# Performance work log

Hardware: AMD Instinct MI355X
Metric: run time of the kernel (lower is better)

## Reference

```python
import jax, jax.numpy as jnp
import numpy as np

N, C, T, V = 32, 64, 512, 25
CO = 64            # out_channels
C4 = CO // 4       # inter channel (conv_a/conv_d output, kc//3)
W3 = 3 * V         # unfolded node dim
BN_EPS = 1e-5


def setup_inputs() -> dict:
    key = jax.random.key(0)
    ks = jax.random.split(key, 12)
    s = 0.05
    return {
        "x": jax.random.normal(ks[0], (N, C, T, V), dtype=jnp.float32),
        "A": jax.random.uniform(ks[1], (3, W3, W3), dtype=jnp.float32) * 0.1,  # fixed adjacency buffer
        "PA": jnp.full((3, W3, W3), 1e-6, dtype=jnp.float32),                   # learned adjacency offset
        "conv_a_w": jax.random.normal(ks[2], (C4, C), dtype=jnp.float32) * s,   # 1x1 conv_a[0]
        "conv_a_b": jnp.zeros((C4,), dtype=jnp.float32),
        "conv_d_w": jax.random.normal(ks[3], (C4, C), dtype=jnp.float32) * s,   # 1x1 conv_d[0]
        "conv_d_b": jnp.zeros((C4,), dtype=jnp.float32),
        "conv_w": jax.random.normal(ks[4], (3 * C4, C), dtype=jnp.float32) * s, # main 1x1 conv (t_kernel_size=1)
        "conv_b": jnp.zeros((3 * C4,), dtype=jnp.float32),
        "out_w": jax.random.normal(ks[5], (CO, C4, 3), dtype=jnp.float32) * s,  # conv3d kernel (1,3,1)
        "out_b": jnp.zeros((CO,), dtype=jnp.float32),
        "bn_gamma": jnp.ones((CO,), dtype=jnp.float32),
        "bn_beta": jnp.zeros((CO,), dtype=jnp.float32),
        "bn_mean": jnp.zeros((CO,), dtype=jnp.float32),
        "bn_var": jnp.ones((CO,), dtype=jnp.float32),
    }


def _unfold3(x):
    # UnfoldTemporalWindows(3,1,1): (N,C,T,V) -> (N,C,T,3V), zero-pad T by 1
    n, c, t, v = x.shape
    xp = jnp.pad(x, ((0, 0), (0, 0), (1, 1), (0, 0)))
    win = jnp.stack([xp[:, :, i:i + t, :] for i in range(3)], axis=3)  # (N,C,T,3,V)
    return win.reshape(n, c, t, 3 * v)


def reference(x, A, PA, conv_a_w, conv_a_b, conv_d_w, conv_d_b,
              conv_w, conv_b, out_w, out_b, bn_gamma, bn_beta, bn_mean, bn_var):
    n, c, t, v = x.shape
    w3 = 3 * v
    Aeff = A + PA  # (3, 3V, 3V)

    x2 = _unfold3(x)  # (N,C,T,3V)

    # adaptive graph attention: matmul-softmax-matmul
    a1 = jnp.einsum('nctw,oc->notw', x2, conv_a_w) + conv_a_b[None, :, None, None]  # (N,C4,T,3V)
    a11 = a1.transpose(0, 3, 1, 2).reshape(n, w3, -1)   # (N,3V,C4*T)
    a2 = a1.reshape(n, -1, w3)                          # (N,C4*T,3V)
    att = jax.nn.softmax(jnp.matmul(a11, a2) / w3, axis=-2)  # (N,3V,3V), softmax over dim -2
    xz = jnp.matmul(x2.reshape(n, c * t, w3), att).reshape(n, c, t, w3)
    z = jnp.einsum('nctw,oc->notw', xz, conv_d_w) + conv_d_b[None, :, None, None]  # (N,C4,T,3V)

    # main branch: 1x1 conv -> split into k=3 -> einsum graph conv with A
    x1 = jnp.einsum('nctw,oc->notw', x2, conv_w) + conv_b[None, :, None, None]  # (N,3*C4,T,3V)
    c4 = conv_d_w.shape[0]
    x1 = x1.reshape(n, 3, c4, t, w3)
    x1 = jnp.einsum('nkctv,kvw->nctw', x1, Aeff)  # (N,C4,T,3V)
    x1 = x1 + z

    # conv3d (1,3,1) collapses the window-of-3 dim
    x1 = x1.reshape(n, c4, t, 3, v)
    y = jnp.einsum('nctwv,ocw->notv', x1, out_w) + out_b[None, :, None, None]  # (N,CO,T,V)

    # BatchNorm2d (inference form)
    inv = jax.lax.rsqrt(bn_var + BN_EPS)
    y = (y - bn_mean[None, :, None, None]) * (bn_gamma * inv)[None, :, None, None] + bn_beta[None, :, None, None]

    y = y + x  # in_channels == out_channels -> identity residual
    return jax.nn.relu(y)
```

## Files before the change

### kernel.cpp

```cpp
#include <hip/hip_runtime.h>
#include <hip/hip_bf16.h>


typedef unsigned short u16;
typedef unsigned int   u32;
typedef __attribute__((ext_vector_type(8))) short bf16x8;
typedef __attribute__((ext_vector_type(4))) float f32x4;

__device__ __forceinline__ float b2f(u32 u) {
    union { u32 i; float f; } x; x.i = (u & 0xffffu) << 16; return x.f;
}
__device__ __forceinline__ u16 f2b(float f) {
    union { float f; u32 i; } x; x.f = f;
    u32 i = x.i;
    return (u16)((i + 0x7fffu + ((i >> 16) & 1u)) >> 16);
}
__device__ __forceinline__ u32 pack2(float a, float b) {
    return (u32)f2b(a) | ((u32)f2b(b) << 16);
}

__global__ __launch_bounds__(256) void k0_bta(
    const float* __restrict__ A, const float* __restrict__ PA,
    u16* __restrict__ BtA)
{
    int e = blockIdx.x * 256 + threadIdx.x;
    if (e >= 80 * 288) return;
    int w = e / 288, k = e - w * 288;
    int r = k >> 5, v = k & 31, g = r / 3, i = r - g * 3;
    float val = 0.f;
    if (v < 25 && w < 75) {
        int idx = (g * 75 + i * 25 + v) * 75 + w;
        val = A[idx] + PA[idx];
    }
    BtA[e] = f2b(val);
}

__global__ __launch_bounds__(256, 2) void k1_conv80(
    const float* __restrict__ x,
    const float* __restrict__ wa, const float* __restrict__ ba,
    const float* __restrict__ wd, const float* __restrict__ bd,
    const float* __restrict__ wc, const float* __restrict__ bc,
    u16* __restrict__ a1o, u16* __restrict__ hcn)
{
    __shared__ __align__(16) u16 Xt[256 * 64];
    __shared__ __align__(16) u16 Csh[80 * 264];
    char* XtB = (char*)Xt;

    const int b    = blockIdx.x;
    const int n    = b >> 4;
    const int t0   = (b & 15) << 5;
    const int tid  = threadIdx.x;
    const int wave = tid >> 6, lane = tid & 63;
    const int q    = lane >> 4, r = lane & 15;

    bf16x8 wfrag[5][2];
    float  breg[5];
    #pragma unroll
    for (int mt = 0; mt < 5; ++mt) {
        const int o = mt * 16 + r;
        const float* src = (o < 16) ? (wa + o * 64)
                         : (o < 32) ? (wd + (o - 16) * 64)
                                    : (wc + (o - 32) * 64);
        breg[mt] = (o < 16) ? ba[o] : (o < 32) ? bd[o - 16] : bc[o - 32];
        #pragma unroll
        for (int ks = 0; ks < 2; ++ks) {
            bf16x8 f;
            #pragma unroll
            for (int j = 0; j < 8; ++j)
                f[j] = (short)f2b(src[ks * 32 + q * 8 + j]);
            wfrag[mt][ks] = f;
        }
    }

    if (t0 == 0) {
        uint4 z; z.x = 0u; z.y = 0u; z.z = 0u; z.w = 0u;
        for (int e = tid; e < 50; e += 256)
            *(uint4*)&a1o[((size_t)n * 514) * 400 + e * 8] = z;
    }
    if (t0 == 480) {
        uint4 z; z.x = 0u; z.y = 0u; z.z = 0u; z.w = 0u;
        for (int e = tid; e < 50; e += 256)
            *(uint4*)&a1o[((size_t)n * 514 + 513) * 400 + e * 8] = z;
    }

    {
        uint4 z; z.x = 0u; z.y = 0u; z.z = 0u; z.w = 0u;
        for (int e = tid; e < 448; e += 256) {
            const int pc = e >> 3, ch = e & 7;
            const int tl = pc / 7, pv = pc - tl * 7;
            const int col = tl * 32 + 25 + pv;
            *(uint4*)(XtB + col * 128 + ch * 16) = z;
        }
    }

    auto epilogue = [&](int tbp) {
        for (int e = tid; e < 2048; e += 256) {
            const int tl  = e >> 8;
            const int rem = e & 255;
            const int cc  = rem >> 2, v0 = (rem & 3) << 3;
            const int o   = (cc < 48) ? cc + 32 : cc - 32;
            uint4 pk = *(const uint4*)&Csh[o * 264 + tl * 32 + v0];
            *(uint4*)&hcn[(((size_t)n * 512 + (tbp + tl)) * 64 + cc) * 32 + v0] = pk;
        }
        for (int e = tid; e < 400; e += 256) {
            const int tv = e >> 1, h = (e & 1) << 3;
            const int tl = (tv * 41) >> 10;
            const int v  = tv - tl * 25;
            const int cb = tl * 32 + v;
            u16 a[8];
            #pragma unroll
            for (int k = 0; k < 8; ++k) a[k] = Csh[(h + k) * 264 + cb];
            uint4 pk;
            pk.x = (u32)a[0] | ((u32)a[1] << 16);
            pk.y = (u32)a[2] | ((u32)a[3] << 16);
            pk.z = (u32)a[4] | ((u32)a[5] << 16);
            pk.w = (u32)a[6] | ((u32)a[7] << 16);
            *(uint4*)&a1o[(((size_t)n * 514 + (tbp + tl + 1)) * 25 + v) * 16 + h] = pk;
        }
    };

    for (int s = 0; s < 4; ++s) {
        const int tb = t0 + s * 8;

        if (s > 0) epilogue(tb - 8);
        for (int e = tid; e < 400; e += 256) {
            const int co = e / 50;
            const int tq = e - co * 50;
            const float* gp = x + (((size_t)n * 64 + co * 8) * 512 + tb) * 25 + tq * 4;
            float fl[32];
            #pragma unroll
            for (int i = 0; i < 8; ++i) {
                const float4 t4 = *(const float4*)(gp + (size_t)i * 12800);
                fl[i * 4 + 0] = t4.x; fl[i * 4 + 1] = t4.y;
                fl[i * 4 + 2] = t4.z; fl[i * 4 + 3] = t4.w;
            }
            #pragma unroll
            for (int j = 0; j < 4; ++j) {
                const int tv  = tq * 4 + j;
                const int tl  = (tv * 41) >> 10;
                const int col = tl * 32 + (tv - tl * 25);
                uint4 pk;
                pk.x = pack2(fl[0 * 4 + j], fl[1 * 4 + j]);
                pk.y = pack2(fl[2 * 4 + j], fl[3 * 4 + j]);
                pk.z = pack2(fl[4 * 4 + j], fl[5 * 4 + j]);
                pk.w = pack2(fl[6 * 4 + j], fl[7 * 4 + j]);
                *(uint4*)(XtB + col * 128 + ((co * 16) ^ ((col & 7) << 4))) = pk;
            }
        }
        __syncthreads();

        {
            f32x4 acc[4][5];
            #pragma unroll
            for (int a_ = 0; a_ < 4; ++a_)
                #pragma unroll
                for (int m_ = 0; m_ < 5; ++m_)
                    acc[a_][m_] = (f32x4){0.f, 0.f, 0.f, 0.f};

            #pragma unroll
            for (int nt4 = 0; nt4 < 4; ++nt4) {
                const int col = (wave * 4 + nt4) * 16 + r;
                const int swz = (col & 7) << 4;
                const char* rowp = (const char*)Xt + col * 128;
                const bf16x8 x0 = *(const bf16x8*)(rowp + ((q * 16) ^ swz));
                const bf16x8 x1 = *(const bf16x8*)(rowp + ((64 + q * 16) ^ swz));
                #pragma unroll
                for (int mt = 0; mt < 5; ++mt) {
                    acc[nt4][mt] = __builtin_amdgcn_mfma_f32_16x16x32_bf16(
                        x0, wfrag[mt][0], acc[nt4][mt], 0, 0, 0);
                    acc[nt4][mt] = __builtin_amdgcn_mfma_f32_16x16x32_bf16(
                        x1, wfrag[mt][1], acc[nt4][mt], 0, 0, 0);
                }
            }
            #pragma unroll
            for (int nt4 = 0; nt4 < 4; ++nt4) {
                const int colb = (wave * 4 + nt4) * 16 + q * 4;
                #pragma unroll
                for (int mt = 0; mt < 5; ++mt) {
                    const int o = mt * 16 + r;
                    const float bi = breg[mt];
                    uint2 pr;
                    pr.x = pack2(acc[nt4][mt][0] + bi, acc[nt4][mt][1] + bi);
                    pr.y = pack2(acc[nt4][mt][2] + bi, acc[nt4][mt][3] + bi);
                    *(uint2*)&Csh[o * 264 + colb] = pr;
                }
            }
        }
        __syncthreads();
    }
    epilogue(t0 + 24);
}

__global__ __launch_bounds__(256, 2) void k2a_mfma(
    const u16* __restrict__ a1o, float* __restrict__ Spart)
{
    __shared__ u16 U[80 * 136];
    __shared__ float Sred[80 * 80];
    __shared__ float Sred2[80 * 80];
    const int b   = blockIdx.x;
    const int n   = b >> 4;
    const int tc  = b & 15;
    const int t0  = tc * 32;
    const int tid = threadIdx.x;
    const int wave = tid >> 6, lane = tid & 63;
    const int q = lane >> 4, col = lane & 15;

    f32x4 acc[25];
    #pragma unroll
    for (int i = 0; i < 25; ++i) acc[i] = (f32x4){0.f, 0.f, 0.f, 0.f};

    for (int s = 0; s < 4; ++s) {
        __syncthreads();
        for (int e = tid; e < 1280; e += 256) {
            int row = e >> 4, c8 = (e & 15) << 3;
            uint4 val; val.x = 0u; val.y = 0u; val.z = 0u; val.w = 0u;
            if (row < 75) {
                int i = row / 25, v = row - i * 25;
                int tl = c8 >> 4, o0 = c8 & 8;
                int tp = t0 + s * 8 + tl + i;
                val = *(const uint4*)&a1o[(((size_t)n * 514 + tp) * 25 + v) * 16 + o0];
            }
            *(uint4*)&U[row * 136 + c8] = val;
        }
        __syncthreads();

        const int k0 = wave * 32 + q * 8;
        bf16x8 fr[5];
        #pragma unroll
        for (int r = 0; r < 5; ++r)
            fr[r] = *(const bf16x8*)&U[(r * 16 + col) * 136 + k0];
        #pragma unroll
        for (int mt = 0; mt < 5; ++mt)
            #pragma unroll
            for (int nt = 0; nt < 5; ++nt)
                acc[mt * 5 + nt] = __builtin_amdgcn_mfma_f32_16x16x32_bf16(
                    fr[mt], fr[nt], acc[mt * 5 + nt], 0, 0, 0);
    }

    if (wave < 2) {
        float* S = (wave == 0) ? Sred : Sred2;
        #pragma unroll
        for (int mt = 0; mt < 5; ++mt)
            #pragma unroll
            for (int nt = 0; nt < 5; ++nt)
                #pragma unroll
                for (int reg = 0; reg < 4; ++reg)
                    S[(mt * 16 + q * 4 + reg) * 80 + nt * 16 + col] =
                        acc[mt * 5 + nt][reg];
    }
    __syncthreads();
    if (wave >= 2) {
        float* S = (wave == 2) ? Sred : Sred2;
        #pragma unroll
        for (int mt = 0; mt < 5; ++mt)
            #pragma unroll
            for (int nt = 0; nt < 5; ++nt)
                #pragma unroll
                for (int reg = 0; reg < 4; ++reg)
                    S[(mt * 16 + q * 4 + reg) * 80 + nt * 16 + col] +=
                        acc[mt * 5 + nt][reg];
    }
    __syncthreads();
    float* dst = &Spart[(size_t)(n * 16 + tc) * 6400];
    for (int e = tid; e < 6400; e += 256) dst[e] = Sred[e] + Sred2[e];
}

__global__ __launch_bounds__(256) void k2b_softmax(
    const float* __restrict__ Spart, u16* __restrict__ BtT)
{
    __shared__ float S2[75][17];
    const int b = blockIdx.x;
    const int n = b / 5, w2g = b - n * 5;
    const int w2base = w2g * 16;
    const int tid = threadIdx.x;

    for (int e = tid; e < 1200; e += 256) {
        const int w1 = e >> 4, w2l = e & 15;
        const float* sp = &Spart[(size_t)(n * 16) * 6400 + w1 * 80 + w2base + w2l];
        float s = 0.f;
        #pragma unroll
        for (int ks = 0; ks < 16; ++ks) s += sp[(size_t)ks * 6400];
        S2[w1][w2l] = s * (1.0f / 75.0f);
    }
    __syncthreads();

    const int w2l = tid >> 4, j = tid & 15;
    float m = -1e30f;
    for (int w1 = j; w1 < 75; w1 += 16) m = fmaxf(m, S2[w1][w2l]);
    #pragma unroll
    for (int off = 8; off; off >>= 1) m = fmaxf(m, __shfl_xor(m, off, 16));
    float s = 0.f;
    for (int w1 = j; w1 < 75; w1 += 16) {
        const float e = __expf(S2[w1][w2l] - m);
        S2[w1][w2l] = e;
        s += e;
    }
    #pragma unroll
    for (int off = 8; off; off >>= 1) s += __shfl_xor(s, off, 16);
    const float r = 1.0f / s;
    for (int w1 = j; w1 < 75; w1 += 16) S2[w1][w2l] *= r;
    __syncthreads();

    for (int e = tid; e < 1536; e += 256) {
        const int wl = e / 96, k = e - wl * 96;
        const int i = k >> 5, v = k & 31;
        const int w2 = w2base + wl;
        const float val = (w2 < 75 && v < 25) ? S2[i * 25 + v][wl] : 0.f;
        BtT[((size_t)n * 80 + w2) * 96 + k] = f2b(val);
    }
}

__global__ __launch_bounds__(256, 2) void k34_fused(
    const u16* __restrict__ hcn, const u16* __restrict__ BtA,
    const u16* __restrict__ BtT,
    const float* __restrict__ ow, const float* __restrict__ obias,
    const float* __restrict__ bg, const float* __restrict__ bb,
    const float* __restrict__ bm, const float* __restrict__ bv,
    const float* __restrict__ x, float* __restrict__ out)
{
    __shared__ __align__(16) char smem[81920];
    u16*   Bt   = (u16*)smem;
    u16*   tile = (u16*)(smem + 62720);
    float* Csh  = (float*)smem;

    const int b    = blockIdx.x;
    const int n    = b >> 6;
    const int t0   = (b & 63) << 3;
    const int tid  = threadIdx.x;
    const int wave = tid >> 6, lane = tid & 63;
    const int q    = lane >> 4, c15 = lane & 15;

    for (int e = tid; e < 3840; e += 256) {
        int row = e / 48, cs = e - row * 48;
        uint4 val;
        if (cs < 36) val = *(const uint4*)&BtA[row * 288 + cs * 8];
        else         val = *(const uint4*)&BtT[((size_t)n * 80 + row) * 96 + (cs - 36) * 8];
        *(uint4*)&Bt[row * 392 + cs * 8] = val;
    }

    const int tp = t0 + 2 * wave;
    bf16x8 frag[4][4];
    #pragma unroll
    for (int g = 0; g < 4; ++g)
        #pragma unroll
        for (int s2 = 0; s2 < 4; ++s2) {
            const int t = tp - 1 + s2;
            frag[g][s2] = (t >= 0 && t < 512)
                ? *(const bf16x8*)&hcn[(((size_t)n * 512 + t) * 64 + g * 16 + c15) * 32 + q * 8]
                : (bf16x8)(short)0;
        }

    bf16x8 wfrag[4][2];
    #pragma unroll
    for (int mt = 0; mt < 4; ++mt) {
        const int o = mt * 16 + c15;
        #pragma unroll
        for (int ks = 0; ks < 2; ++ks) {
            bf16x8 f;
            #pragma unroll
            for (int j = 0; j < 8; ++j) {
                const int k = ks * 32 + q * 8 + j;
                const int cc = k & 15, ww = k >> 4;
                f[j] = (k < 48) ? (short)f2b(ow[o * 48 + cc * 3 + ww]) : (short)0;
            }
            wfrag[mt][ks] = f;
        }
    }
    float scl[4][4], shf2[4][4];
    #pragma unroll
    for (int mt = 0; mt < 4; ++mt)
        #pragma unroll
        for (int reg = 0; reg < 4; ++reg) {
            const int o = mt * 16 + q * 4 + reg;
            const float s = bg[o] * rsqrtf(bv[o] + 1e-5f);
            scl[mt][reg]  = s;
            shf2[mt][reg] = bb[o] + (obias[o] - bm[o]) * s;
        }
    __syncthreads();

    #pragma unroll 1
    for (int nt = 0; nt < 5; ++nt) {
        f32x4 acc0 = {0.f, 0.f, 0.f, 0.f};
        f32x4 acc1 = {0.f, 0.f, 0.f, 0.f};
        const u16* bp = &Bt[(nt * 16 + c15) * 392 + q * 8];
        #pragma unroll
        for (int g = 0; g < 4; ++g)
            #pragma unroll
            for (int i = 0; i < 3; ++i) {
                bf16x8 bf = *(const bf16x8*)(bp + (g * 3 + i) * 32);
                acc0 = __builtin_amdgcn_mfma_f32_16x16x32_bf16(bf, frag[g][i],     acc0, 0, 0, 0);
                acc1 = __builtin_amdgcn_mfma_f32_16x16x32_bf16(bf, frag[g][i + 1], acc1, 0, 0, 0);
            }
        #pragma unroll
        for (int reg = 0; reg < 4; ++reg) {
            const int w = nt * 16 + q * 4 + reg;
            if (w < 75) {
                const int ww = (w >= 50) ? 2 : ((w >= 25) ? 1 : 0);
                const int v  = w - ww * 25;
                const int off = (v * 3 + ww) * 16 + c15;
                tile[(2 * wave)     * 1200 + off] = f2b(acc0[reg]);
                tile[(2 * wave + 1) * 1200 + off] = f2b(acc1[reg]);
            }
        }
    }
    __syncthreads();

    f32x4 acc[4][4];
    #pragma unroll
    for (int ct = 0; ct < 4; ++ct)
        #pragma unroll
        for (int mt = 0; mt < 4; ++mt)
            acc[ct][mt] = (f32x4){0.f, 0.f, 0.f, 0.f};

    const int wb = wave * 64;
    const int ww0 = q >> 1, cs2 = (q & 1) * 8;
    #pragma unroll
    for (int ct = 0; ct < 4; ++ct) {
        const int col = wb + ct * 16 + c15;
        const int tl = col >> 5, v = col & 31;
        const int vv = (v < 25) ? v : 0;
        const u16* trow = tile + tl * 1200;
        const bf16x8 b0 = *(const bf16x8*)&trow[(vv * 3 + ww0) * 16 + cs2];
        const bf16x8 b1 = *(const bf16x8*)&trow[(vv * 3 + 2) * 16 + cs2];
        #pragma unroll
        for (int mt = 0; mt < 4; ++mt) {
            acc[ct][mt] = __builtin_amdgcn_mfma_f32_16x16x32_bf16(
                wfrag[mt][0], b0, acc[ct][mt], 0, 0, 0);
            acc[ct][mt] = __builtin_amdgcn_mfma_f32_16x16x32_bf16(
                wfrag[mt][1], b1, acc[ct][mt], 0, 0, 0);
        }
    }

    #pragma unroll
    for (int ct = 0; ct < 4; ++ct) {
        const int col = wb + ct * 16 + c15;
        const int tl = col >> 5, v = col & 31;
        if (v < 25) {
            const int cc = tl * 25 + v;
            #pragma unroll
            for (int mt = 0; mt < 4; ++mt)
                #pragma unroll
                for (int reg = 0; reg < 4; ++reg) {
                    const int o = mt * 16 + q * 4 + reg;
                    Csh[o * 204 + cc] =
                        acc[ct][mt][reg] * scl[mt][reg] + shf2[mt][reg];
                }
        }
    }
    __syncthreads();

    for (int e = tid; e < 3200; e += 256) {
        const int o = e / 50, jj = e - o * 50;
        const size_t gidx = (((size_t)n * 64 + o) * 512 + t0) * 25 + jj * 4;
        const float4 xv = *(const float4*)&x[gidx];
        const float* cp = &Csh[o * 204 + jj * 4];
        float4 yv;
        yv.x = fmaxf(cp[0] + xv.x, 0.f);
        yv.y = fmaxf(cp[1] + xv.y, 0.f);
        yv.z = fmaxf(cp[2] + xv.z, 0.f);
        yv.w = fmaxf(cp[3] + xv.w, 0.f);
        *(float4*)&out[gidx] = yv;
    }
}

extern "C" void kernel_launch(void* const* d_in, const int* in_sizes, int n_in,
                              void* d_out, int out_size, void* d_ws, size_t ws_size,
                              hipStream_t stream)
{
    const float* x  = (const float*)d_in[0];
    const float* A  = (const float*)d_in[1];
    const float* PA = (const float*)d_in[2];
    const float* wa = (const float*)d_in[3];
    const float* ba = (const float*)d_in[4];
    const float* wd = (const float*)d_in[5];
    const float* bd = (const float*)d_in[6];
    const float* wc = (const float*)d_in[7];
    const float* bc = (const float*)d_in[8];
    const float* ow = (const float*)d_in[9];
    const float* ob = (const float*)d_in[10];
    const float* bg = (const float*)d_in[11];
    const float* bb = (const float*)d_in[12];
    const float* bm = (const float*)d_in[13];
    const float* bv = (const float*)d_in[14];
    float* out = (float*)d_out;

    char* ws = (char*)d_ws;
    u16*   a1o   = (u16*)(ws);
    u16*   hcn   = (u16*)(ws + 13158400);
    float* Spart = (float*)(ws + 80267264);
    u16*   BtA   = (u16*)(ws + 130598912);
    u16*   BtT   = (u16*)(ws + 130644992);

    k0_bta    <<<90,   256, 0, stream>>>(A, PA, BtA);
    k1_conv80 <<<512,  256, 0, stream>>>(x, wa, ba, wd, bd, wc, bc, a1o, hcn);
    k2a_mfma  <<<512,  256, 0, stream>>>(a1o, Spart);
    k2b_softmax<<<160, 256, 0, stream>>>(Spart, BtT);
    k34_fused <<<2048, 256, 0, stream>>>(hcn, BtA, BtT, ow, ob, bg, bb, bm, bv, x, out);
}
```

Before: 377.5 us.

## Pre-pack adjacency/attention B fragments and load them directly from global in k34

The A+PA and softmax attention matrices are now written in an MFMA-fragment-packed layout, so k34_fused reads B fragments straight from global/L2 into registers instead of staging them through a 62KB LDS tile. This cuts LDS to about 52KB and raises launch bounds to 3 blocks per CU for more occupancy. Weight fragment and BN constant loads are moved later to lower register pressure, and the accumulation is split into two chains to add MFMA ILP. The cost is repeated global loads of B per wave and a tighter register budget.

```diff
diff --git a/kernel.cpp b/kernel.cpp
--- a/kernel.cpp
+++ b/kernel.cpp
@@ -21,18 +21,23 @@
 
 __global__ __launch_bounds__(256) void k0_bta(
     const float* __restrict__ A, const float* __restrict__ PA,
-    u16* __restrict__ BtA)
+    u16* __restrict__ BtApck)
 {
     int e = blockIdx.x * 256 + threadIdx.x;
-    if (e >= 80 * 288) return;
-    int w = e / 288, k = e - w * 288;
-    int r = k >> 5, v = k & 31, g = r / 3, i = r - g * 3;
+    if (e >= 23040) return;
+    const int nt  = e / 4608;
+    const int rem = e - nt * 4608;
+    const int r   = rem >> 9;
+    const int c   = (rem >> 5) & 15;
+    const int v   = rem & 31;
+    const int w   = nt * 16 + c;
+    const int g   = r / 3, i = r - g * 3;
     float val = 0.f;
     if (v < 25 && w < 75) {
         int idx = (g * 75 + i * 25 + v) * 75 + w;
         val = A[idx] + PA[idx];
     }
-    BtA[e] = f2b(val);
+    BtApck[e] = f2b(val);
 }
 
 __global__ __launch_bounds__(256, 2) void k1_conv80(
@@ -266,7 +271,7 @@
 }
 
 __global__ __launch_bounds__(256) void k2b_softmax(
-    const float* __restrict__ Spart, u16* __restrict__ BtT)
+    const float* __restrict__ Spart, u16* __restrict__ BtTp)
 {
     __shared__ float S2[75][17];
     const int b = blockIdx.x;
@@ -302,25 +307,25 @@
     __syncthreads();
 
     for (int e = tid; e < 1536; e += 256) {
-        const int wl = e / 96, k = e - wl * 96;
-        const int i = k >> 5, v = k & 31;
-        const int w2 = w2base + wl;
-        const float val = (w2 < 75 && v < 25) ? S2[i * 25 + v][wl] : 0.f;
-        BtT[((size_t)n * 80 + w2) * 96 + k] = f2b(val);
-    }
-}
-
-__global__ __launch_bounds__(256, 2) void k34_fused(
-    const u16* __restrict__ hcn, const u16* __restrict__ BtA,
-    const u16* __restrict__ BtT,
+        const int i = e >> 9;
+        const int c = (e >> 5) & 15;
+        const int v = e & 31;
+        const int w2 = w2base + c;
+        const float val = (w2 < 75 && v < 25) ? S2[i * 25 + v][c] : 0.f;
+        BtTp[((size_t)n * 5 + w2g) * 1536 + e] = f2b(val);
+    }
+}
+
+__global__ __launch_bounds__(256, 3) void k34_fused(
+    const u16* __restrict__ hcn, const u16* __restrict__ BtApck,
+    const u16* __restrict__ BtTp,
     const float* __restrict__ ow, const float* __restrict__ obias,
     const float* __restrict__ bg, const float* __restrict__ bb,
     const float* __restrict__ bm, const float* __restrict__ bv,
     const float* __restrict__ x, float* __restrict__ out)
 {
-    __shared__ __align__(16) char smem[81920];
-    u16*   Bt   = (u16*)smem;
-    u16*   tile = (u16*)(smem + 62720);
+    __shared__ __align__(16) char smem[52224];
+    u16*   tile = (u16*)smem;
     float* Csh  = (float*)smem;
 
     const int b    = blockIdx.x;
@@ -330,14 +335,6 @@
     const int wave = tid >> 6, lane = tid & 63;
     const int q    = lane >> 4, c15 = lane & 15;
 
-    for (int e = tid; e < 3840; e += 256) {
-        int row = e / 48, cs = e - row * 48;
-        uint4 val;
-        if (cs < 36) val = *(const uint4*)&BtA[row * 288 + cs * 8];
-        else         val = *(const uint4*)&BtT[((size_t)n * 80 + row) * 96 + (cs - 36) * 8];
-        *(uint4*)&Bt[row * 392 + cs * 8] = val;
-    }
-
     const int tp = t0 + 2 * wave;
     bf16x8 frag[4][4];
     #pragma unroll
@@ -350,47 +347,35 @@
                 : (bf16x8)(short)0;
         }
 
-    bf16x8 wfrag[4][2];
-    #pragma unroll
-    for (int mt = 0; mt < 4; ++mt) {
-        const int o = mt * 16 + c15;
-        #pragma unroll
-        for (int ks = 0; ks < 2; ++ks) {
-            bf16x8 f;
-            #pragma unroll
-            for (int j = 0; j < 8; ++j) {
-                const int k = ks * 32 + q * 8 + j;
-                const int cc = k & 15, ww = k >> 4;
-                f[j] = (k < 48) ? (short)f2b(ow[o * 48 + cc * 3 + ww]) : (short)0;
-            }
-            wfrag[mt][ks] = f;
-        }
-    }
-    float scl[4][4], shf2[4][4];
-    #pragma unroll
-    for (int mt = 0; mt < 4; ++mt)
-        #pragma unroll
-        for (int reg = 0; reg < 4; ++reg) {
-            const int o = mt * 16 + q * 4 + reg;
-            const float s = bg[o] * rsqrtf(bv[o] + 1e-5f);
-            scl[mt][reg]  = s;
-            shf2[mt][reg] = bb[o] + (obias[o] - bm[o]) * s;
-        }
-    __syncthreads();
-
+    const int lofs = (c15 * 4 + q) * 8;
+    const u16* btTn = BtTp + (size_t)n * 5 * 1536;
     #pragma unroll 1
     for (int nt = 0; nt < 5; ++nt) {
-        f32x4 acc0 = {0.f, 0.f, 0.f, 0.f};
-        f32x4 acc1 = {0.f, 0.f, 0.f, 0.f};
-        const u16* bp = &Bt[(nt * 16 + c15) * 392 + q * 8];
+        bf16x8 bfr[12];
+        #pragma unroll
+        for (int r = 0; r < 9; ++r)
+            bfr[r] = *(const bf16x8*)&BtApck[(nt * 9 + r) * 512 + lofs];
+        #pragma unroll
+        for (int i = 0; i < 3; ++i)
+            bfr[9 + i] = *(const bf16x8*)&btTn[nt * 1536 + i * 512 + lofs];
+
+        f32x4 a0a = {0.f,0.f,0.f,0.f}, a0b = {0.f,0.f,0.f,0.f};
+        f32x4 a1a = {0.f,0.f,0.f,0.f}, a1b = {0.f,0.f,0.f,0.f};
         #pragma unroll
         for (int g = 0; g < 4; ++g)
             #pragma unroll
             for (int i = 0; i < 3; ++i) {
-                bf16x8 bf = *(const bf16x8*)(bp + (g * 3 + i) * 32);
-                acc0 = __builtin_amdgcn_mfma_f32_16x16x32_bf16(bf, frag[g][i],     acc0, 0, 0, 0);
-                acc1 = __builtin_amdgcn_mfma_f32_16x16x32_bf16(bf, frag[g][i + 1], acc1, 0, 0, 0);
-            }
+                const int r = g * 3 + i;
+                if (r < 6) {
+                    a0a = __builtin_amdgcn_mfma_f32_16x16x32_bf16(bfr[r], frag[g][i],     a0a, 0, 0, 0);
+                    a1a = __builtin_amdgcn_mfma_f32_16x16x32_bf16(bfr[r], frag[g][i + 1], a1a, 0, 0, 0);
+                } else {
+                    a0b = __builtin_amdgcn_mfma_f32_16x16x32_bf16(bfr[r], frag[g][i],     a0b, 0, 0, 0);
+                    a1b = __builtin_amdgcn_mfma_f32_16x16x32_bf16(bfr[r], frag[g][i + 1], a1b, 0, 0, 0);
+                }
+            }
+        const f32x4 acc0 = a0a + a0b;
+        const f32x4 acc1 = a1a + a1b;
         #pragma unroll
         for (int reg = 0; reg < 4; ++reg) {
             const int w = nt * 16 + q * 4 + reg;
@@ -405,6 +390,23 @@
     }
     __syncthreads();
 
+    bf16x8 wfrag[4][2];
+    #pragma unroll
+    for (int mt = 0; mt < 4; ++mt) {
+        const int o = mt * 16 + c15;
+        #pragma unroll
+        for (int ks = 0; ks < 2; ++ks) {
+            bf16x8 f;
+            #pragma unroll
+            for (int j = 0; j < 8; ++j) {
+                const int k = ks * 32 + q * 8 + j;
+                const int cc = k & 15, ww = k >> 4;
+                f[j] = (k < 48) ? (short)f2b(ow[o * 48 + cc * 3 + ww]) : (short)0;
+            }
+            wfrag[mt][ks] = f;
+        }
+    }
+
     f32x4 acc[4][4];
     #pragma unroll
     for (int ct = 0; ct < 4; ++ct)
@@ -430,7 +432,18 @@
                 wfrag[mt][1], b1, acc[ct][mt], 0, 0, 0);
         }
     }
-
+    __syncthreads();
+
+    float scl[4][4], shf2[4][4];
+    #pragma unroll
+    for (int mt = 0; mt < 4; ++mt)
+        #pragma unroll
+        for (int reg = 0; reg < 4; ++reg) {
+            const int o = mt * 16 + q * 4 + reg;
+            const float s = bg[o] * rsqrtf(bv[o] + 1e-5f);
+            scl[mt][reg]  = s;
+            shf2[mt][reg] = bb[o] + (obias[o] - bm[o]) * s;
+        }
     #pragma unroll
     for (int ct = 0; ct < 4; ++ct) {
         const int col = wb + ct * 16 + c15;
@@ -485,15 +498,15 @@
     float* out = (float*)d_out;
 
     char* ws = (char*)d_ws;
-    u16*   a1o   = (u16*)(ws);
-    u16*   hcn   = (u16*)(ws + 13158400);
-    float* Spart = (float*)(ws + 80267264);
-    u16*   BtA   = (u16*)(ws + 130598912);
-    u16*   BtT   = (u16*)(ws + 130644992);
-
-    k0_bta    <<<90,   256, 0, stream>>>(A, PA, BtA);
+    u16*   a1o    = (u16*)(ws);
+    u16*   hcn    = (u16*)(ws + 13158400);
+    float* Spart  = (float*)(ws + 80267264);
+    u16*   BtApck = (u16*)(ws + 130598912);
+    u16*   BtTp   = (u16*)(ws + 130644992);
+
+    k0_bta    <<<90,   256, 0, stream>>>(A, PA, BtApck);
     k1_conv80 <<<512,  256, 0, stream>>>(x, wa, ba, wd, bd, wc, bc, a1o, hcn);
     k2a_mfma  <<<512,  256, 0, stream>>>(a1o, Spart);
-    k2b_softmax<<<160, 256, 0, stream>>>(Spart, BtT);
-    k34_fused <<<2048, 256, 0, stream>>>(hcn, BtA, BtT, ow, ob, bg, bb, bm, bv, x, out);
-}
+    k2b_softmax<<<160, 256, 0, stream>>>(Spart, BtTp);
+    k34_fused <<<2048, 256, 0, stream>>>(hcn, BtApck, BtTp, ow, ob, bg, bb, bm, bv, x, out);
+}
```

Result: slower. 386.0 us (+2.3%).
